# Performance work log

Hardware: AMD Instinct MI355X
Metric: run time of the kernel (lower is better)

Reference implementation:

```python
import jax, jax.numpy as jnp
import numpy as np

N = 50000        # num_nodes
E = 800000       # num edges (avg degree 16)
IN = 512         # embedding_dim[0]
H = 128          # hidden_dim = embedding_dim[1]
C = 64           # out_dim = n_classes = embedding_dim[-1]
L = 3            # layer_num = len(embedding_dim) - 1


def _lin(k, fan_in, fan_out):
    s = 1.0 / np.sqrt(fan_in)
    k1, k2 = jax.random.split(k)
    W = jax.random.uniform(k1, (fan_in, fan_out), jnp.float32, -s, s)
    b = jax.random.uniform(k2, (fan_out,), jnp.float32, -s, s)
    return W, b


def setup_inputs() -> dict:
    key = jax.random.key(0)
    ks = jax.random.split(key, 12)
    d = {}
    d["x"] = jax.random.normal(ks[0], (N, IN), jnp.float32)
    d["edge_index"] = jax.random.randint(ks[1], (2, E), 0, N)
    # pseudo_mlp: in_dim -> 512 -> 64 -> out_dim
    d["Wp1"], d["bp1"] = _lin(ks[2], IN, 512)
    d["Wp2"], d["bp2"] = _lin(ks[3], 512, 64)
    d["Wp3"], d["bp3"] = _lin(ks[4], 64, C)
    # parsing_mats[0] (only ln=0 is used in learn_soft_edge3), init ones/scaling_factor
    d["parsing0"] = jnp.ones((C, C), jnp.float32) / 2.0 + 0.01 * jax.random.normal(ks[5], (C, C), jnp.float32)
    # GCNConv weights (PyG style: linear without bias, bias added after aggregation)
    d["Wg0"], d["bg0"] = _lin(ks[6], IN, H)
    d["Wg1"], d["bg1"] = _lin(ks[7], H, H)
    d["Wg2"], d["bg2"] = _lin(ks[8], H, H)
    # JK 'cat' -> lin1 input is (layer_num-1)*hidden
    d["Wl1"], d["bl1"] = _lin(ks[9], (L - 1) * H, H)
    d["Wl2"], d["bl2"] = _lin(ks[10], H, C)
    return d


def gcn_conv(x, W, b, edge_index, ew, n):
    """PyG GCNConv with per-edge weight ew, add_self_loops=True (loop weight 1)."""
    xw = x @ W                                           # [N, F_out]
    row, col = edge_index[0], edge_index[1]
    loop = jnp.arange(n)
    row2 = jnp.concatenate([row, loop])
    col2 = jnp.concatenate([col, loop])
    ew2 = jnp.concatenate([ew, jnp.ones((n,), xw.dtype)])
    deg = jax.ops.segment_sum(ew2, col2, num_segments=n)
    dis = jnp.where(deg > 0, jax.lax.rsqrt(deg), 0.0)    # deg^-1/2, inf -> 0
    norm = dis[row2] * ew2 * dis[col2]                   # [E+N]
    out = jax.ops.segment_sum(norm[:, None] * xw[row2], col2, num_segments=n)
    return out + b


def soft_edge_weight(x, edge_index, Wp1, bp1, Wp2, bp2, Wp3, bp3, parsing0):
    """learn_soft_edge3: bilinear form start^T * relu(2*P) * end per edge.
    Original materializes an [E,C,C] outer product then bmm + diagonal; the
    diagonal-sum equals einsum('ek,ed,dk->e', start, end, parsing), computed
    here as a fused small matmul + elementwise reduce (same math)."""
    h = jax.nn.relu(x @ Wp1 + bp1)
    h = jax.nn.relu(h @ Wp2 + bp2)
    logits = h @ Wp3 + bp3                               # [N, C]
    parsing = jax.nn.relu(2.0 * parsing0)                # scaling_factor = 2
    s = logits[edge_index[0]]                            # [E, C] start
    e = logits[edge_index[1]]                            # [E, C] end
    ew = jnp.sum((e @ parsing) * s, axis=-1)             # [E]
    mean = ew.mean()
    var = jnp.var(ew, ddof=1)                            # torch .var() is unbiased
    return (ew - mean) * jnp.sqrt(1e-4 / var) + 1.0


def reference(x, edge_index, Wp1, bp1, Wp2, bp2, Wp3, bp3, parsing0,
              Wg0, bg0, Wg1, bg1, Wg2, bg2, Wl1, bl1, Wl2, bl2):
    n = x.shape[0]
    ew = soft_edge_weight(x, edge_index, Wp1, bp1, Wp2, bp2, Wp3, bp3, parsing0)
    # layer 0
    x1 = jax.nn.relu(gcn_conv(x, Wg0, bg0, edge_index, ew, n))
    xs = [x1]
    # ln = 1 (not last): conv -> relu -> (dropout off in eval) -> append
    x2 = jax.nn.relu(gcn_conv(x1, Wg1, bg1, edge_index, ew, n))
    xs.append(x2)
    # ln = 2 (last layer): computed in original but loop breaks before append;
    # jump(xs) overwrites x, so the last conv's output never reaches the output.
    xj = jnp.concatenate(xs, axis=-1)                    # JK 'cat' -> [N, (L-1)*H]
    out = jax.nn.relu(xj @ Wl1 + bl1)
    out = out @ Wl2 + bl2                                # [N, C]
    return out
```

## Files before the change

kernel.cpp:

```cpp
#include <hip/hip_runtime.h>
#include <hip/hip_bf16.h>
#include <cmath>
#include <cstring>

#define NNODES 50000
#define NEDGES 800000
#define IND    512
#define HD     128
#define CD     64

typedef __bf16 bf16x8 __attribute__((ext_vector_type(8)));
typedef float  f32x4  __attribute__((ext_vector_type(4)));
typedef const __attribute__((address_space(1))) unsigned int* gu32p;
typedef __attribute__((address_space(3))) unsigned int* lu32p;

static const size_t XJ_B   = 0;
static const size_t HID_B  = 25600000;
static const size_t H1_B   = 51200000;
static const size_t XW_B   = 102400000;
static const size_t H2_B   = 115200000;
static const size_t LG_B   = 121600000;
static const size_t PE_B   = 128000000;
static const size_t WT_B   = 134400000;
static const size_t CSRR_B = 135300000;
static const size_t EWC_B  = 138500000;
static const size_t CSRW_B = 141700000;
static const size_t CNT_B  = 144900000;
static const size_t S_B    = 145100000;
static const size_t ZERO_BYTES = 200016;
static const size_t RP_B   = 145100016;
static const size_t WOFF_B = 145300020;
static const size_t INCL_B = 145500020;
static const size_t BSUM_B = 145700020;
static const size_t ST_B   = 145701044;
static const size_t DIS_B  = 145701052;

static const size_t WP1T_O = 0;
static const size_t WG0T_O = 524288;
static const size_t WP2T_O = 655360;
static const size_t WP3T_O = 720896;
static const size_t W2T_O  = 729088;
static const size_t WG1T_O = 737280;
static const size_t WL1T_O = 770048;
static const size_t WL2T_O = 835584;
static const size_t BG1_O  = 851968;
static const size_t BG3_O  = 854528;

struct WD { const float* s; __hip_bfloat16* d; int K; int N; };
struct PrepArgs {
    const float* x; __hip_bfloat16* xb;
    WD w[7];
    int bo[8];
    const float* Wp3; const float* bp3; const float* P0; const float* bp1;
    __hip_bfloat16* W2t; float* bias_g1; float* bias_g3;
};
#define PREP_CAST_BLKS 12500
#define PREP_TP_BLKS   1648
#define PREP_BLKS      (PREP_CAST_BLKS + PREP_TP_BLKS + 20)

__global__ __launch_bounds__(256) void prep_all(PrepArgs a)
{
    int b = blockIdx.x;
    int t = threadIdx.x;
    if (b < PREP_CAST_BLKS) {
        int i = b * 256 + t;
        const float4* p = (const float4*)a.x + (size_t)i * 2;
        float4 u = p[0], v = p[1];
        __hip_bfloat16 o[8] __attribute__((aligned(16)));
        o[0] = __float2bfloat16(u.x); o[1] = __float2bfloat16(u.y);
        o[2] = __float2bfloat16(u.z); o[3] = __float2bfloat16(u.w);
        o[4] = __float2bfloat16(v.x); o[5] = __float2bfloat16(v.y);
        o[6] = __float2bfloat16(v.z); o[7] = __float2bfloat16(v.w);
        *(int4*)(a.xb + (size_t)i * 8) = *(const int4*)o;
        return;
    }
    b -= PREP_CAST_BLKS;
    if (b < PREP_TP_BLKS) {
        int m = 0;
        #pragma unroll
        for (int q = 1; q < 7; q++) if (b >= a.bo[q]) m = q;
        WD d = a.w[m];
        int i = (b - a.bo[m]) * 256 + t;
        if (i < d.K * d.N) {
            int k = i % d.K, n = i / d.K;
            d.d[i] = __float2bfloat16(d.s[(size_t)k * d.N + n]);
        }
        return;
    }
    b -= PREP_TP_BLKS;
    if (b < 16) {
        int i = b * 256 + t;
        int k = i >> 6, n = i & 63;
        float s = 0.f;
        for (int j = 0; j < 64; j++)
            s += a.Wp3[k * 64 + j] * fmaxf(2.f * a.P0[j * 64 + n], 0.f);
        a.W2t[n * 64 + k] = __float2bfloat16(s);
    } else if (b == 16) {
        int n = t;
        if (n < 64) {
            float s = 0.f;
            for (int j = 0; j < 64; j++)
                s += a.bp3[j] * fmaxf(2.f * a.P0[j * 64 + n], 0.f);
            a.bias_g3[n] = a.bp3[n];
            a.bias_g3[64 + n] = s;
        }
    } else {
        int i = (b - 17) * 256 + t;
        if (i < 512) a.bias_g1[i] = a.bp1[i];
        else if (i < 640) a.bias_g1[i] = 0.f;
    }
}

template<int BN, int WN>
__global__ __launch_bounds__(256) void gemm_mfma(
    const __hip_bfloat16* __restrict__ Ab, int lda,
    const __hip_bfloat16* __restrict__ Bt, int ldb,
    const float* __restrict__ bias,
    void* __restrict__ Cout, int ldc,
    void* __restrict__ Cout2, int ldc2, int splitN,
    int M, int K, int do_relu, int out_bf16)
{
    constexpr int BF = WN / 16;
    constexpr int BPASS = BN / 64;
    __shared__ __bf16 As[2][128 * 32];
    __shared__ __bf16 Bs[2][BN * 32];

    const int NC = gridDim.x, NR = gridDim.y;
    int g = blockIdx.y * NC + blockIdx.x;
    int per = NC * 8;
    int nfull = (NR >> 3) * per;
    int rowt, colt;
    if (g < nfull) {
        int grp = g / per, rem = g % per;
        rowt = grp * 8 + (rem & 7);
        colt = rem >> 3;
    } else {
        int rem = g - nfull;
        int tail = NR - (NR >> 3) * 8;
        rowt = (NR >> 3) * 8 + rem % tail;
        colt = rem / tail;
    }

    const int t = threadIdx.x;
    const int row0 = rowt * 128;
    const int col0 = colt * BN;

    const int wv   = t >> 6;
    const int lane = t & 63;
    const int quad = lane >> 4;
    const int l16  = lane & 15;
    const int wrow = (wv >> 1) * 64;
    const int wcol = (wv & 1) * WN;

    const int subrow = lane >> 2;
    const int kchunk = (lane & 3) ^ (subrow & 3);
    const int subkg  = kchunk * 8;

    f32x4 acc[4][BF] = {};

    auto stage = [&](int buf, int k0) {
        #pragma unroll
        for (int p = 0; p < 2; p++) {
            int rowA = (p * 4 + wv) * 16 + subrow;
            const __hip_bfloat16* gp = Ab + (size_t)(row0 + rowA) * lda + k0 + subkg;
            __builtin_amdgcn_global_load_lds((gu32p)(const void*)gp,
                (lu32p)(void*)&As[buf][(p * 4 + wv) * 512], 16, 0, 0);
        }
        #pragma unroll
        for (int p = 0; p < BPASS; p++) {
            int rowB = (p * 4 + wv) * 16 + subrow;
            const __hip_bfloat16* gp = Bt + (size_t)(col0 + rowB) * ldb + k0 + subkg;
            __builtin_amdgcn_global_load_lds((gu32p)(const void*)gp,
                (lu32p)(void*)&Bs[buf][(p * 4 + wv) * 512], 16, 0, 0);
        }
    };

    auto compute = [&](int buf) {
        bf16x8 af[4], bfr[BF];
        #pragma unroll
        for (int i = 0; i < 4; i++) {
            int R = wrow + i * 16 + l16;
            af[i] = *(const bf16x8*)&As[buf][R * 32 + ((quad ^ (R & 3)) * 8)];
        }
        #pragma unroll
        for (int j = 0; j < BF; j++) {
            int R = wcol + j * 16 + l16;
            bfr[j] = *(const bf16x8*)&Bs[buf][R * 32 + ((quad ^ (R & 3)) * 8)];
        }
        #pragma unroll
        for (int i = 0; i < 4; i++)
            #pragma unroll
            for (int j = 0; j < BF; j++)
                acc[i][j] = __builtin_amdgcn_mfma_f32_16x16x32_bf16(af[i], bfr[j], acc[i][j], 0, 0, 0);
    };

    const int NT = K >> 5;
    stage(0, 0);
    __syncthreads();
    for (int tt = 0; tt < NT; tt += 2) {
        if (tt + 1 < NT) stage(1, (tt + 1) << 5);
        compute(0);
        if (tt + 1 < NT) __syncthreads(); else break;
        if (tt + 2 < NT) stage(0, (tt + 2) << 5);
        compute(1);
        if (tt + 2 < NT) __syncthreads();
    }

    #pragma unroll
    for (int i = 0; i < 4; i++) {
        #pragma unroll
        for (int j = 0; j < BF; j++) {
            int n = col0 + wcol + j * 16 + l16;
            bool second = (n >= splitN);
            float bv = bias ? bias[n] : 0.f;
            #pragma unroll
            for (int reg = 0; reg < 4; reg++) {
                int m = row0 + wrow + i * 16 + quad * 4 + reg;
                if (m >= M) continue;
                float v = acc[i][j][reg] + bv;
                if (do_relu && !second) v = fmaxf(v, 0.f);
                if (second)
                    ((__hip_bfloat16*)Cout2)[(size_t)m * ldc2 + (n - splitN)] = __float2bfloat16(v);
                else if (out_bf16)
                    ((__hip_bfloat16*)Cout)[(size_t)m * ldc + n] = __float2bfloat16(v);
                else
                    ((float*)Cout)[(size_t)m * ldc + n] = v;
            }
        }
    }
}

__global__ __launch_bounds__(256) void count_kernel(
    const int* __restrict__ ei, int* __restrict__ cnt)
{
    int e = blockIdx.x * 256 + threadIdx.x;
    if (e >= NEDGES) return;
    atomicAdd(&cnt[ei[NEDGES + e]], 1);
}

__global__ __launch_bounds__(256) void scan1_kernel(
    const int* __restrict__ cnt, int* __restrict__ incl, int* __restrict__ bsum)
{
    __shared__ int s[256];
    int t = threadIdx.x;
    int i = blockIdx.x * 256 + t;
    int v = (i < NNODES) ? cnt[i] : 0;
    s[t] = v;
    __syncthreads();
    for (int off = 1; off < 256; off <<= 1) {
        int u = (t >= off) ? s[t - off] : 0;
        __syncthreads();
        s[t] += u;
        __syncthreads();
    }
    if (i < NNODES) incl[i] = s[t];
    if (t == 255) bsum[blockIdx.x] = s[255];
}

__global__ __launch_bounds__(256) void scan3_kernel(
    const int* __restrict__ cnt, const int* __restrict__ incl,
    const int* __restrict__ bsum, int* __restrict__ rowptr,
    int* __restrict__ woff, int nb)
{
    __shared__ int s[256];
    int t = threadIdx.x;
    int v = (t < nb) ? bsum[t] : 0;
    s[t] = v;
    __syncthreads();
    for (int off = 1; off < 256; off <<= 1) {
        int u = (t >= off) ? s[t - off] : 0;
        __syncthreads();
        s[t] += u;
        __syncthreads();
    }
    int off = s[blockIdx.x] - bsum[blockIdx.x];
    int i = blockIdx.x * 256 + t;
    if (i >= NNODES) return;
    int r = incl[i] - cnt[i] + off;
    rowptr[i] = r;
    woff[i] = r;
    if (i == NNODES - 1) rowptr[NNODES] = incl[i] + off;
}

__global__ __launch_bounds__(256) void scatter_idx_kernel(
    const int* __restrict__ ei, int* __restrict__ woff,
    int* __restrict__ csr_row, int* __restrict__ csr_col)
{
    int e = blockIdx.x * 256 + threadIdx.x;
    if (e >= NEDGES) return;
    int r = ei[e];
    int c = ei[NEDGES + e];
    int p = atomicAdd(&woff[c], 1);
    csr_row[p] = r;
    csr_col[p] = c;
}

__global__ __launch_bounds__(256) void edge_ew_gather(
    const __hip_bfloat16* __restrict__ lg, const __hip_bfloat16* __restrict__ pe,
    const int* __restrict__ csr_row, const int* __restrict__ csr_col,
    float* __restrict__ ew_csr)
{
    const int tid = threadIdx.x;
    const int sub = tid & 7;
    const int e = blockIdx.x * 32 + (tid >> 3);
    if (e >= NEDGES) return;
    int r = csr_row[e];
    int c = csr_col[e];
    bf16x8 a = *(const bf16x8*)(lg + (size_t)r * CD + sub * 8);
    bf16x8 b = *(const bf16x8*)(pe + (size_t)c * CD + sub * 8);
    float acc = 0.f;
    #pragma unroll
    for (int u = 0; u < 8; u++)
        acc += (float)a[u] * (float)b[u];
    acc += __shfl_xor(acc, 1);
    acc += __shfl_xor(acc, 2);
    acc += __shfl_xor(acc, 4);
    if (sub == 0) ew_csr[e] = acc;
}

__global__ __launch_bounds__(256) void ew_stats_kernel(
    const float* __restrict__ ew, double* __restrict__ S)
{
    const int tid = threadIdx.x;
    double s1 = 0.0, s2 = 0.0;
    for (int i = blockIdx.x * 256 + tid; i < NEDGES; i += gridDim.x * 256) {
        float v = ew[i];
        s1 += v; s2 += (double)v * (double)v;
    }
    __shared__ double sh1[256], sh2[256];
    sh1[tid] = s1; sh2[tid] = s2;
    __syncthreads();
    for (int s = 128; s > 0; s >>= 1) {
        if (tid < s) { sh1[tid] += sh1[tid + s]; sh2[tid] += sh2[tid + s]; }
        __syncthreads();
    }
    if (tid == 0) {
        atomicAdd(&S[0], sh1[0]);
        atomicAdd(&S[1], sh2[0]);
    }
}

__global__ __launch_bounds__(256) void norm_deg_kernel(
    const int* __restrict__ rowptr, float* __restrict__ ew_csr,
    const double* __restrict__ S, float* __restrict__ dis)
{
    int n = blockIdx.x * 256 + threadIdx.x;
    if (n >= NNODES) return;
    const double Ed = (double)NEDGES;
    double meand = S[0] / Ed;
    double var = (S[1] - S[0] * S[0] / Ed) / (Ed - 1.0);
    float mean = (float)meand;
    float alpha = (float)sqrt(1e-4 / var);
    int s = rowptr[n], e = rowptr[n + 1];
    float sum = 0.f;
    for (int j = s; j < e; j++) {
        float w = (ew_csr[j] - mean) * alpha + 1.0f;
        ew_csr[j] = w;
        sum += w;
    }
    float d = sum + 1.0f;
    dis[n] = (d > 0.f) ? rsqrtf(d) : 0.f;
}

__global__ __launch_bounds__(256) void csrw_kernel(
    const int* __restrict__ rowptr, const int* __restrict__ csr_row,
    const float* __restrict__ ew_csr, const float* __restrict__ dis,
    float* __restrict__ csr_w)
{
    int n = blockIdx.x * 256 + threadIdx.x;
    if (n >= NNODES) return;
    float dn = dis[n];
    int s = rowptr[n], e = rowptr[n + 1];
    for (int j = s; j < e; j++)
        csr_w[j] = dis[csr_row[j]] * ew_csr[j] * dn;
}

__global__ __launch_bounds__(128) void agg_kernel(
    const unsigned* __restrict__ xw32, const float* __restrict__ dis,
    const int* __restrict__ rowptr, const int* __restrict__ csr_row,
    const float* __restrict__ csr_w, const float* __restrict__ bias,
    __hip_bfloat16* __restrict__ out, int ldo)
{
    const int wv = threadIdx.x >> 6, lane = threadIdx.x & 63;
    const int n = blockIdx.x * 2 + wv;
    if (n >= NNODES) return;
    float dn = dis[n];
    unsigned v0 = xw32[(size_t)n * 64 + lane];
    float aL = dn * dn * __uint_as_float(v0 << 16);
    float aH = dn * dn * __uint_as_float(v0 & 0xffff0000u);
    int s = rowptr[n], e = rowptr[n + 1];
    int j = s;
    for (; j + 4 <= e; j += 4) {
        int r0 = csr_row[j], r1 = csr_row[j + 1];
        int r2 = csr_row[j + 2], r3 = csr_row[j + 3];
        float w0 = csr_w[j], w1 = csr_w[j + 1];
        float w2 = csr_w[j + 2], w3 = csr_w[j + 3];
        unsigned g0 = xw32[(size_t)r0 * 64 + lane];
        unsigned g1 = xw32[(size_t)r1 * 64 + lane];
        unsigned g2 = xw32[(size_t)r2 * 64 + lane];
        unsigned g3 = xw32[(size_t)r3 * 64 + lane];
        aL = fmaf(w0, __uint_as_float(g0 << 16), aL);
        aH = fmaf(w0, __uint_as_float(g0 & 0xffff0000u), aH);
        aL = fmaf(w1, __uint_as_float(g1 << 16), aL);
        aH = fmaf(w1, __uint_as_float(g1 & 0xffff0000u), aH);
        aL = fmaf(w2, __uint_as_float(g2 << 16), aL);
        aH = fmaf(w2, __uint_as_float(g2 & 0xffff0000u), aH);
        aL = fmaf(w3, __uint_as_float(g3 << 16), aL);
        aH = fmaf(w3, __uint_as_float(g3 & 0xffff0000u), aH);
    }
    for (; j < e; j++) {
        int r = csr_row[j];
        float w = csr_w[j];
        unsigned g = xw32[(size_t)r * 64 + lane];
        aL = fmaf(w, __uint_as_float(g << 16), aL);
        aH = fmaf(w, __uint_as_float(g & 0xffff0000u), aH);
    }
    float2 b = *(const float2*)(bias + 2 * lane);
    aL = fmaxf(aL + b.x, 0.f);
    aH = fmaxf(aH + b.y, 0.f);
    __hip_bfloat16 bl = __float2bfloat16(aL), bh = __float2bfloat16(aH);
    unsigned short ul, uh;
    memcpy(&ul, &bl, 2); memcpy(&uh, &bh, 2);
    unsigned o = (unsigned)ul | ((unsigned)uh << 16);
    *(unsigned*)(out + (size_t)n * ldo + 2 * lane) = o;
}

extern "C" void kernel_launch(void* const* d_in, const int* in_sizes, int n_in,
                              void* d_out, int out_size, void* d_ws, size_t ws_size,
                              hipStream_t stream)
{
    const float* x   = (const float*)d_in[0];
    const int*   ei  = (const int*)d_in[1];
    const float* Wp1 = (const float*)d_in[2];
    const float* bp1 = (const float*)d_in[3];
    const float* Wp2 = (const float*)d_in[4];
    const float* bp2 = (const float*)d_in[5];
    const float* Wp3 = (const float*)d_in[6];
    const float* bp3 = (const float*)d_in[7];
    const float* P0  = (const float*)d_in[8];
    const float* Wg0 = (const float*)d_in[9];
    const float* bg0 = (const float*)d_in[10];
    const float* Wg1 = (const float*)d_in[11];
    const float* bg1 = (const float*)d_in[12];
    const float* Wl1 = (const float*)d_in[15];
    const float* bl1 = (const float*)d_in[16];
    const float* Wl2 = (const float*)d_in[17];
    const float* bl2 = (const float*)d_in[18];
    float* out = (float*)d_out;

    char* wsb = (char*)d_ws;
    __hip_bfloat16* xj     = (__hip_bfloat16*)(wsb + XJ_B);
    __hip_bfloat16* xb16   = (__hip_bfloat16*)(wsb + XJ_B);
    __hip_bfloat16* hid    = (__hip_bfloat16*)(wsb + HID_B);
    __hip_bfloat16* h1     = (__hip_bfloat16*)(wsb + H1_B);
    __hip_bfloat16* xw     = (__hip_bfloat16*)(wsb + XW_B);
    __hip_bfloat16* h2     = (__hip_bfloat16*)(wsb + H2_B);
    __hip_bfloat16* lg     = (__hip_bfloat16*)(wsb + LG_B);
    __hip_bfloat16* pe     = (__hip_bfloat16*)(wsb + PE_B);
    int*            csr_row= (int*)(wsb + CSRR_B);
    float*          ew_csr = (float*)(wsb + EWC_B);
    int*            csr_col= (int*)(wsb + CSRW_B);
    float*          csr_w  = (float*)(wsb + CSRW_B);
    int*            cnt    = (int*)(wsb + CNT_B);
    double*         S      = (double*)(wsb + S_B);
    int*            rowptr = (int*)(wsb + RP_B);
    int*            woff   = (int*)(wsb + WOFF_B);
    int*            incl   = (int*)(wsb + INCL_B);
    int*            bsum   = (int*)(wsb + BSUM_B);
    float*          dis    = (float*)(wsb + DIS_B);

    __hip_bfloat16* Wp1t = (__hip_bfloat16*)(wsb + WT_B + WP1T_O);
    __hip_bfloat16* Wg0t = (__hip_bfloat16*)(wsb + WT_B + WG0T_O);
    __hip_bfloat16* Wp2t = (__hip_bfloat16*)(wsb + WT_B + WP2T_O);
    __hip_bfloat16* Wp3t = (__hip_bfloat16*)(wsb + WT_B + WP3T_O);
    __hip_bfloat16* W2t  = (__hip_bfloat16*)(wsb + WT_B + W2T_O);
    __hip_bfloat16* Wg1t = (__hip_bfloat16*)(wsb + WT_B + WG1T_O);
    __hip_bfloat16* Wl1t = (__hip_bfloat16*)(wsb + WT_B + WL1T_O);
    __hip_bfloat16* Wl2t = (__hip_bfloat16*)(wsb + WT_B + WL2T_O);
    float*          bias_g1 = (float*)(wsb + WT_B + BG1_O);
    float*          bias_g3 = (float*)(wsb + WT_B + BG3_O);

    const int EB = (NEDGES + 255) / 256;
    const int NB = (NNODES + 255) / 256;
    const int MT = (NNODES + 127) / 128;
    const int BIGN = 1 << 30;

    hipMemsetAsync(wsb + CNT_B, 0, ZERO_BYTES, stream);

    PrepArgs pa;
    pa.x = x; pa.xb = xb16;
    pa.w[0] = { Wp1, Wp1t, 512, 512 };
    pa.w[1] = { Wg0, Wg0t, 512, 128 };
    pa.w[2] = { Wp2, Wp2t, 512,  64 };
    pa.w[3] = { Wp3, Wp3t,  64,  64 };
    pa.w[4] = { Wg1, Wg1t, 128, 128 };
    pa.w[5] = { Wl1, Wl1t, 256, 128 };
    pa.w[6] = { Wl2, Wl2t, 128,  64 };
    pa.bo[0] = 0;    pa.bo[1] = 1024; pa.bo[2] = 1280; pa.bo[3] = 1408;
    pa.bo[4] = 1424; pa.bo[5] = 1488; pa.bo[6] = 1616; pa.bo[7] = 1648;
    pa.Wp3 = Wp3; pa.bp3 = bp3; pa.P0 = P0; pa.bp1 = bp1;
    pa.W2t = W2t; pa.bias_g1 = bias_g1; pa.bias_g3 = bias_g3;
    prep_all<<<PREP_BLKS, 256, 0, stream>>>(pa);

    count_kernel<<<EB, 256, 0, stream>>>(ei, cnt);
    scan1_kernel<<<NB, 256, 0, stream>>>(cnt, incl, bsum);
    scan3_kernel<<<NB, 256, 0, stream>>>(cnt, incl, bsum, rowptr, woff, NB);
    scatter_idx_kernel<<<EB, 256, 0, stream>>>(ei, woff, csr_row, csr_col);

    gemm_mfma<128, 64><<<dim3(5, MT), 256, 0, stream>>>(
        xb16, 512, Wp1t, 512, bias_g1, h1, 512, xw, 128, 512, NNODES, 512, 1, 1);

    gemm_mfma<64, 32><<<dim3(1, MT), 256, 0, stream>>>(
        h1, 512, Wp2t, 512, bp2, h2, 64, nullptr, 0, BIGN, NNODES, 512, 1, 1);

    gemm_mfma<128, 64><<<dim3(1, MT), 256, 0, stream>>>(
        h2, 64, Wp3t, 64, bias_g3, lg, 64, pe, 64, 64, NNODES, 64, 0, 1);

    edge_ew_gather<<<(NEDGES + 31) / 32, 256, 0, stream>>>(lg, pe, csr_row, csr_col, ew_csr);
    ew_stats_kernel<<<512, 256, 0, stream>>>(ew_csr, S);
    norm_deg_kernel<<<NB, 256, 0, stream>>>(rowptr, ew_csr, S, dis);
    csrw_kernel<<<NB, 256, 0, stream>>>(rowptr, csr_row, ew_csr, dis, csr_w);

    agg_kernel<<<25000, 128, 0, stream>>>((const unsigned*)xw, dis, rowptr, csr_row, csr_w, bg0, xj, 2 * HD);

    gemm_mfma<64, 32><<<dim3(2, MT), 256, 0, stream>>>(
        xj, 2 * HD, Wg1t, 128, nullptr, xw, 128, nullptr, 0, BIGN, NNODES, 128, 0, 1);
    agg_kernel<<<25000, 128, 0, stream>>>((const unsigned*)xw, dis, rowptr, csr_row, csr_w, bg1, xj + HD, 2 * HD);

    gemm_mfma<128, 64><<<dim3(1, MT), 256, 0, stream>>>(
        xj, 2 * HD, Wl1t, 256, bl1, hid, 128, nullptr, 0, BIGN, NNODES, 256, 1, 1);
    gemm_mfma<64, 32><<<dim3(1, MT), 256, 0, stream>>>(
        hid, 128, Wl2t, 128, bl2, out, 64, nullptr, 0, BIGN, NNODES, 128, 0, 0);
}
```

Measured before the change: 591.4 us.

## Parametrize GEMM row tile and drop LDS double buffering for smaller tiles

Adds a BM template parameter so the smaller GEMMs (pseudo-MLP layers 2/3, GCN layer 1, JK linear layers) run with 64-row tiles and twice as many blocks. The K loop changes from a double-buffered LDS pipeline to a single buffer with a sync before and after each compute step. The aim is better occupancy and CU coverage on the narrow GEMMs, plus half the LDS per block. The cost is that global-to-LDS loads no longer overlap with MFMA work, including on the large first GEMM.

```diff
diff --git a/kernel.cpp b/kernel.cpp
--- a/kernel.cpp
+++ b/kernel.cpp
@@ -111,7 +111,7 @@
     }
 }
 
-template<int BN, int WN>
+template<int BM, int BN, int WN>
 __global__ __launch_bounds__(256) void gemm_mfma(
     const __hip_bfloat16* __restrict__ Ab, int lda,
     const __hip_bfloat16* __restrict__ Bt, int ldb,
@@ -121,9 +121,11 @@
     int M, int K, int do_relu, int out_bf16)
 {
     constexpr int BF = WN / 16;
+    constexpr int MI = BM / 32;
+    constexpr int APASS = BM / 64;
     constexpr int BPASS = BN / 64;
-    __shared__ __bf16 As[2][128 * 32];
-    __shared__ __bf16 Bs[2][BN * 32];
+    __shared__ __bf16 As[BM * 32];
+    __shared__ __bf16 Bs[BN * 32];
 
     const int NC = gridDim.x, NR = gridDim.y;
     int g = blockIdx.y * NC + blockIdx.x;
@@ -142,72 +144,60 @@
     }
 
     const int t = threadIdx.x;
-    const int row0 = rowt * 128;
+    const int row0 = rowt * BM;
     const int col0 = colt * BN;
 
     const int wv   = t >> 6;
     const int lane = t & 63;
     const int quad = lane >> 4;
     const int l16  = lane & 15;
-    const int wrow = (wv >> 1) * 64;
+    const int wrow = (wv >> 1) * (BM / 2);
     const int wcol = (wv & 1) * WN;
 
     const int subrow = lane >> 2;
     const int kchunk = (lane & 3) ^ (subrow & 3);
     const int subkg  = kchunk * 8;
 
-    f32x4 acc[4][BF] = {};
-
-    auto stage = [&](int buf, int k0) {
-        #pragma unroll
-        for (int p = 0; p < 2; p++) {
+    f32x4 acc[MI][BF] = {};
+
+    for (int k0 = 0; k0 < K; k0 += 32) {
+        #pragma unroll
+        for (int p = 0; p < APASS; p++) {
             int rowA = (p * 4 + wv) * 16 + subrow;
             const __hip_bfloat16* gp = Ab + (size_t)(row0 + rowA) * lda + k0 + subkg;
             __builtin_amdgcn_global_load_lds((gu32p)(const void*)gp,
-                (lu32p)(void*)&As[buf][(p * 4 + wv) * 512], 16, 0, 0);
+                (lu32p)(void*)&As[(p * 4 + wv) * 512], 16, 0, 0);
         }
         #pragma unroll
         for (int p = 0; p < BPASS; p++) {
             int rowB = (p * 4 + wv) * 16 + subrow;
             const __hip_bfloat16* gp = Bt + (size_t)(col0 + rowB) * ldb + k0 + subkg;
             __builtin_amdgcn_global_load_lds((gu32p)(const void*)gp,
-                (lu32p)(void*)&Bs[buf][(p * 4 + wv) * 512], 16, 0, 0);
-        }
-    };
-
-    auto compute = [&](int buf) {
-        bf16x8 af[4], bfr[BF];
-        #pragma unroll
-        for (int i = 0; i < 4; i++) {
+                (lu32p)(void*)&Bs[(p * 4 + wv) * 512], 16, 0, 0);
+        }
+        __syncthreads();
+
+        bf16x8 af[MI], bfr[BF];
+        #pragma unroll
+        for (int i = 0; i < MI; i++) {
             int R = wrow + i * 16 + l16;
-            af[i] = *(const bf16x8*)&As[buf][R * 32 + ((quad ^ (R & 3)) * 8)];
+            af[i] = *(const bf16x8*)&As[R * 32 + ((quad ^ (R & 3)) * 8)];
         }
         #pragma unroll
         for (int j = 0; j < BF; j++) {
             int R = wcol + j * 16 + l16;
-            bfr[j] = *(const bf16x8*)&Bs[buf][R * 32 + ((quad ^ (R & 3)) * 8)];
-        }
-        #pragma unroll
-        for (int i = 0; i < 4; i++)
+            bfr[j] = *(const bf16x8*)&Bs[R * 32 + ((quad ^ (R & 3)) * 8)];
+        }
+        #pragma unroll
+        for (int i = 0; i < MI; i++)
             #pragma unroll
             for (int j = 0; j < BF; j++)
                 acc[i][j] = __builtin_amdgcn_mfma_f32_16x16x32_bf16(af[i], bfr[j], acc[i][j], 0, 0, 0);
-    };
-
-    const int NT = K >> 5;
-    stage(0, 0);
-    __syncthreads();
-    for (int tt = 0; tt < NT; tt += 2) {
-        if (tt + 1 < NT) stage(1, (tt + 1) << 5);
-        compute(0);
-        if (tt + 1 < NT) __syncthreads(); else break;
-        if (tt + 2 < NT) stage(0, (tt + 2) << 5);
-        compute(1);
-        if (tt + 2 < NT) __syncthreads();
+        __syncthreads();
     }
 
     #pragma unroll
-    for (int i = 0; i < 4; i++) {
+    for (int i = 0; i < MI; i++) {
         #pragma unroll
         for (int j = 0; j < BF; j++) {
             int n = col0 + wcol + j * 16 + l16;
@@ -482,7 +472,8 @@
 
     const int EB = (NEDGES + 255) / 256;
     const int NB = (NNODES + 255) / 256;
-    const int MT = (NNODES + 127) / 128;
+    const int MT  = (NNODES + 127) / 128;
+    const int MT64 = (NNODES + 63) / 64;
     const int BIGN = 1 << 30;
 
     hipMemsetAsync(wsb + CNT_B, 0, ZERO_BYTES, stream);
@@ -507,13 +498,13 @@
     scan3_kernel<<<NB, 256, 0, stream>>>(cnt, incl, bsum, rowptr, woff, NB);
     scatter_idx_kernel<<<EB, 256, 0, stream>>>(ei, woff, csr_row, csr_col);
 
-    gemm_mfma<128, 64><<<dim3(5, MT), 256, 0, stream>>>(
+    gemm_mfma<128, 128, 64><<<dim3(5, MT), 256, 0, stream>>>(
         xb16, 512, Wp1t, 512, bias_g1, h1, 512, xw, 128, 512, NNODES, 512, 1, 1);
 
-    gemm_mfma<64, 32><<<dim3(1, MT), 256, 0, stream>>>(
+    gemm_mfma<64, 64, 32><<<dim3(1, MT64), 256, 0, stream>>>(
         h1, 512, Wp2t, 512, bp2, h2, 64, nullptr, 0, BIGN, NNODES, 512, 1, 1);
 
-    gemm_mfma<128, 64><<<dim3(1, MT), 256, 0, stream>>>(
+    gemm_mfma<64, 128, 64><<<dim3(1, MT64), 256, 0, stream>>>(
         h2, 64, Wp3t, 64, bias_g3, lg, 64, pe, 64, 64, NNODES, 64, 0, 1);
 
     edge_ew_gather<<<(NEDGES + 31) / 32, 256, 0, stream>>>(lg, pe, csr_row, csr_col, ew_csr);
@@ -523,12 +514,12 @@
 
     agg_kernel<<<25000, 128, 0, stream>>>((const unsigned*)xw, dis, rowptr, csr_row, csr_w, bg0, xj, 2 * HD);
 
-    gemm_mfma<64, 32><<<dim3(2, MT), 256, 0, stream>>>(
+    gemm_mfma<64, 64, 32><<<dim3(2, MT64), 256, 0, stream>>>(
         xj, 2 * HD, Wg1t, 128, nullptr, xw, 128, nullptr, 0, BIGN, NNODES, 128, 0, 1);
     agg_kernel<<<25000, 128, 0, stream>>>((const unsigned*)xw, dis, rowptr, csr_row, csr_w, bg1, xj + HD, 2 * HD);
 
-    gemm_mfma<128, 64><<<dim3(1, MT), 256, 0, stream>>>(
+    gemm_mfma<64, 64, 32><<<dim3(2, MT64), 256, 0, stream>>>(
         xj, 2 * HD, Wl1t, 256, bl1, hid, 128, nullptr, 0, BIGN, NNODES, 256, 1, 1);
-    gemm_mfma<64, 32><<<dim3(1, MT), 256, 0, stream>>>(
+    gemm_mfma<64, 64, 32><<<dim3(1, MT64), 256, 0, stream>>>(
         hid, 128, Wl2t, 128, bl2, out, 64, nullptr, 0, BIGN, NNODES, 128, 0, 0);
 }
```

Result: faster. 543.5 us (-8.1%).
